# Optimization experiments

Measured on AMD Instinct MI355X. Metric: run time of the kernel, lower is better.

## Reference

```python
import jax, jax.numpy as jnp
import numpy as np

HID, H, D, DFF = 128, 4, 128, 2048   # hidden_dim, nheads, out_feats per head, dim_feedforward
N, E, B = 32768, 524288, 32
EPS = 1e-5
SLOPE = 0.2  # DGL EdgeGATConv negative_slope default


def setup_inputs() -> dict:
    key = jax.random.key(0)
    ks = jax.random.split(key, 16)
    s = 0.05
    return {
        "h": jax.random.normal(ks[0], (N, HID), jnp.float32),
        "e": jax.random.normal(ks[1], (E, 1), jnp.float32),
        "src": jax.random.randint(ks[2], (E,), 0, N, jnp.int32),
        "dst": jax.random.randint(ks[3], (E,), 0, N, jnp.int32),
        "batch_size": B,
        # EdgeGATConv params (fc / fc_edge / res_fc are bias-free in DGL)
        "W_fc": jax.random.normal(ks[4], (HID, H * D), jnp.float32) * s,
        "attn_l": jax.random.normal(ks[5], (H, D), jnp.float32) * s,
        "attn_r": jax.random.normal(ks[6], (H, D), jnp.float32) * s,
        "W_fe": jax.random.normal(ks[7], (1, H * D), jnp.float32) * s,
        "attn_e": jax.random.normal(ks[8], (H, D), jnp.float32) * s,
        "W_res": jax.random.normal(ks[9], (HID, H * D), jnp.float32) * s,
        "gat_bias": jnp.zeros((H * D,), jnp.float32),
        # linear_mha + norms + FFN
        "W_mha": jax.random.normal(ks[10], (H * D, HID), jnp.float32) * s,
        "b_mha": jnp.zeros((HID,), jnp.float32),
        "n1_g": jnp.ones((HID,), jnp.float32),
        "n1_b": jnp.zeros((HID,), jnp.float32),
        "n2_g": jnp.ones((HID,), jnp.float32),
        "n2_b": jnp.zeros((HID,), jnp.float32),
        "W1": jax.random.normal(ks[11], (HID, DFF), jnp.float32) * s,
        "b1": jnp.zeros((DFF,), jnp.float32),
        "W2": jax.random.normal(ks[12], (DFF, HID), jnp.float32) * s,
        "b2": jnp.zeros((HID,), jnp.float32),
    }


def _ln(x, g, b):
    mu = x.mean(-1, keepdims=True)
    var = ((x - mu) ** 2).mean(-1, keepdims=True)
    return (x - mu) * jax.lax.rsqrt(var + EPS) * g + b


def reference(h, e, src, dst, batch_size, W_fc, attn_l, attn_r, W_fe, attn_e,
              W_res, gat_bias, W_mha, b_mha, n1_g, n1_b, n2_g, n2_b,
              W1, b1, W2, b2):
    n = h.shape[0]
    h0 = h
    # --- EdgeGATConv (eval mode: dropouts are identity) ---
    ft = (h @ W_fc).reshape(n, H, D)                         # (N,H,D)
    el = jnp.einsum("nhd,hd->nh", ft, attn_l)                # (N,H)
    er = jnp.einsum("nhd,hd->nh", ft, attn_r)
    fe = (e @ W_fe).reshape(-1, H, D)                        # (E,H,D)
    ee = jnp.einsum("ehd,hd->eh", fe, attn_e)                # (E,H)
    sc = jax.nn.leaky_relu(el[src] + er[dst] + ee, SLOPE)    # (E,H)
    # segment softmax over incoming edges of each dst node
    m = jax.ops.segment_max(sc, dst, num_segments=n)         # (N,H)
    m = jnp.where(jnp.isfinite(m), m, 0.0)                   # empty segments
    w = jnp.exp(sc - m[dst])
    z = jax.ops.segment_sum(w, dst, num_segments=n)
    zd = z[dst]
    alpha = w / jnp.where(zd == 0, 1.0, zd)                  # (E,H)
    msg = ft[src] * alpha[:, :, None]                        # (E,H,D)
    rst = jax.ops.segment_sum(msg, dst, num_segments=n)      # (N,H,D)
    rst = rst + (h0 @ W_res).reshape(n, H, D) + gat_bias.reshape(1, H, D)
    # --- transformer wrapper ---
    x = jax.nn.relu(rst).reshape(n, H * D)
    x = jax.nn.relu(x @ W_mha + b_mha)
    x = _ln(h0 + x, n1_g, n1_b)
    x = x.reshape(batch_size, -1, x.shape[1])                # (B, N/B, HID)
    ff = jax.nn.relu(x @ W1 + b1) @ W2 + b2
    return _ln(x + ff, n2_g, n2_b)
```

## Files before the change

kernel.cpp:

```cpp
#include <hip/hip_runtime.h>
#include <hip/hip_bf16.h>

#define N_NODES 32768
#define E_EDGES 524288
#define HIDDIM 128
#define FDIM 512
#define DFF 2048
#define LN_EPS 1e-5f
#define SLOPE 0.2f
#define CAP 64

typedef __bf16 bf16_t;
typedef __bf16 bf16x8 __attribute__((ext_vector_type(8)));
typedef float f32x4 __attribute__((ext_vector_type(4)));
typedef float f32x2 __attribute__((ext_vector_type(2)));

#define GLD_LDS16(gp, lp) __builtin_amdgcn_global_load_lds( \
    (const __attribute__((address_space(1))) unsigned int*)(gp), \
    (__attribute__((address_space(3))) unsigned int*)(lp), 16, 0, 0)

__device__ inline unsigned char f32_to_e4m3(float v) {
#if __has_builtin(__builtin_amdgcn_cvt_pk_fp8_f32)
    return (unsigned char)(__builtin_amdgcn_cvt_pk_fp8_f32(v, v, 0, false) & 0xff);
#else
    unsigned bits = __float_as_uint(v);
    unsigned sign = (bits >> 24) & 0x80;
    float av = fabsf(v);
    if (av >= 448.f) return (unsigned char)(sign | 0x7E);
    int e = (int)((bits >> 23) & 0xFF) - 127;
    if (e < -6) { int n = (int)rintf(av * 512.f); return (unsigned char)(sign | n); }
    float ulp = exp2f((float)(e - 3));
    int n = (int)rintf(av / ulp);
    if (n == 16) { e += 1; n = 8; }
    return (unsigned char)(sign | ((e + 7) << 3) | (n - 8));
#endif
}
template<bool HI>
__device__ inline f32x2 e4m3x2_to_f32(unsigned u) {
#if __has_builtin(__builtin_amdgcn_cvt_pk_f32_fp8)
    return __builtin_amdgcn_cvt_pk_f32_fp8(u, HI);
#else
    f32x2 r;
    unsigned b0 = HI ? ((u >> 16) & 0xff) : (u & 0xff);
    unsigned b1 = HI ? ((u >> 24) & 0xff) : ((u >> 8) & 0xff);
    unsigned bs[2] = {b0, b1};
    for (int i = 0; i < 2; ++i) {
        unsigned b = bs[i];
        float s = (b & 0x80) ? -1.f : 1.f;
        int e = (b >> 3) & 15, m = b & 7;
        float v = e ? (8 + m) * exp2f((float)(e - 10)) : m * exp2f(-9.f);
        r[i] = s * v;
    }
    return r;
#endif
}

__device__ inline void pack_range(const float* __restrict__ B, bf16_t* __restrict__ out,
                                  int id, int N) {
    const int g = id / N, n = id % N;
    union { bf16_t b[8]; uint4 u; } pk;
#pragma unroll
    for (int j = 0; j < 8; ++j) pk.b[j] = (bf16_t)B[(size_t)(g * 8 + j) * N + n];
    *(uint4*)(out + (size_t)id * 8) = pk.u;
}

__global__ __launch_bounds__(256) void prep_kernel(const float* __restrict__ h, bf16_t* __restrict__ hb,
                                                   const float* __restrict__ W_fc, bf16_t* __restrict__ Wfc_p,
                                                   const float* __restrict__ W_res, bf16_t* __restrict__ Wres_p,
                                                   const float* __restrict__ W_mha, bf16_t* __restrict__ Wmha_p,
                                                   const float* __restrict__ W1, bf16_t* __restrict__ W1_p,
                                                   const float* __restrict__ W2, bf16_t* __restrict__ W2_p,
                                                   const float* __restrict__ W_fe, const float* __restrict__ attn_e,
                                                   float* __restrict__ ce) {
    int bid = blockIdx.x;
    const int tid = threadIdx.x;
    if (bid < 4096) {
        const int id = bid * 256 + tid;
        const float4 v = ((const float4*)h)[id];
        union { bf16_t b[4]; uint2 u; } pk;
        pk.b[0] = (bf16_t)v.x; pk.b[1] = (bf16_t)v.y; pk.b[2] = (bf16_t)v.z; pk.b[3] = (bf16_t)v.w;
        *(uint2*)(hb + (size_t)id * 4) = pk.u;
        return;
    }
    bid -= 4096;
    if (bid < 32)  { pack_range(W_fc,  Wfc_p,  bid * 256 + tid, 512);  return; }
    bid -= 32;
    if (bid < 32)  { pack_range(W_res, Wres_p, bid * 256 + tid, 512);  return; }
    bid -= 32;
    if (bid < 32)  { pack_range(W_mha, Wmha_p, bid * 256 + tid, 128);  return; }
    bid -= 32;
    if (bid < 128) { pack_range(W1,    W1_p,   bid * 256 + tid, 2048); return; }
    bid -= 128;
    if (bid < 128) { pack_range(W2,    W2_p,   bid * 256 + tid, 128);  return; }
    if (tid < 128) {
        const float4 w = ((const float4*)W_fe)[tid];
        const float4 a = ((const float4*)attn_e)[tid];
        float p = w.x * a.x + w.y * a.y + w.z * a.z + w.w * a.w;
        for (int off = 16; off; off >>= 1) p += __shfl_down(p, off, 32);
        if ((tid & 31) == 0) ce[tid >> 5] = p;
    }
}

__global__ __launch_bounds__(256, 2) void gemm_ftres(const bf16_t* __restrict__ A,
                                                     const bf16_t* __restrict__ Bf,
                                                     const bf16_t* __restrict__ Brs,
                                                     const float* __restrict__ attn_l,
                                                     const float* __restrict__ attn_r,
                                                     unsigned char* __restrict__ ft8,
                                                     float* __restrict__ el,
                                                     float* __restrict__ er,
                                                     bf16_t* __restrict__ res) {
    __shared__ __align__(16) bf16_t lA[4096];
    __shared__ __align__(16) bf16_t lBf[4096];
    __shared__ __align__(16) bf16_t lBr[4096];
    __shared__ float s_el[2][128], s_er[2][128];
    const int tid = threadIdx.x, lane = tid & 63, wave = tid >> 6;
    const int wm = (wave >> 1) * 64, wn = (wave & 1) * 64;
    const int row0 = blockIdx.y * 128;
    const int head = blockIdx.x, col0 = head * 128;
    const int ko = lane >> 4, rl = lane & 15;
    f32x4 accf[4][4] = {};
    f32x4 accr[4][4] = {};
    const int c0 = tid, c1 = tid + 256;
    const int g0 = c0 >> 7, m0 = c0 & 127;
    const int g1 = c1 >> 7, m1 = c1 & 127;
    for (int k0 = 0; k0 < 128; k0 += 32) {
        __syncthreads();
        GLD_LDS16(A + (size_t)(row0 + m0) * 128 + k0 + g0 * 8, lA + c0 * 8);
        GLD_LDS16(A + (size_t)(row0 + m1) * 128 + k0 + g1 * 8, lA + c1 * 8);
        GLD_LDS16(Bf + ((size_t)(k0 / 8 + g0) * 512 + col0 + m0) * 8, lBf + c0 * 8);
        GLD_LDS16(Bf + ((size_t)(k0 / 8 + g1) * 512 + col0 + m1) * 8, lBf + c1 * 8);
        GLD_LDS16(Brs + ((size_t)(k0 / 8 + g0) * 512 + col0 + m0) * 8, lBr + c0 * 8);
        GLD_LDS16(Brs + ((size_t)(k0 / 8 + g1) * 512 + col0 + m1) * 8, lBr + c1 * 8);
        __syncthreads();
        bf16x8 af[4], bff[4], bfr[4];
#pragma unroll
        for (int i = 0; i < 4; ++i) {
            af[i]  = *(const bf16x8*)&lA[(ko * 128 + wm + i * 16 + rl) * 8];
            bff[i] = *(const bf16x8*)&lBf[(ko * 128 + wn + i * 16 + rl) * 8];
            bfr[i] = *(const bf16x8*)&lBr[(ko * 128 + wn + i * 16 + rl) * 8];
        }
#pragma unroll
        for (int i = 0; i < 4; ++i)
#pragma unroll
            for (int j = 0; j < 4; ++j) {
                accf[i][j] = __builtin_amdgcn_mfma_f32_16x16x32_bf16(af[i], bff[j], accf[i][j], 0, 0, 0);
                accr[i][j] = __builtin_amdgcn_mfma_f32_16x16x32_bf16(af[i], bfr[j], accr[i][j], 0, 0, 0);
            }
    }
    const int cr = (lane >> 4) * 4, cc = lane & 15;
    float al[4], ar[4];
#pragma unroll
    for (int j = 0; j < 4; ++j) {
        al[j] = attn_l[col0 + wn + j * 16 + cc];
        ar[j] = attn_r[col0 + wn + j * 16 + cc];
    }
#pragma unroll
    for (int i = 0; i < 4; ++i)
#pragma unroll
        for (int r = 0; r < 4; ++r) {
            const int row = row0 + wm + i * 16 + cr + r;
            float pel = 0.f, per = 0.f;
#pragma unroll
            for (int j = 0; j < 4; ++j) {
                const int col = col0 + wn + j * 16 + cc;
                const float v = accf[i][j][r];
                ft8[(size_t)row * 512 + col] = f32_to_e4m3(v);
                res[(size_t)row * 512 + col] = (bf16_t)accr[i][j][r];
                pel += v * al[j];
                per += v * ar[j];
            }
#pragma unroll
            for (int m = 1; m < 16; m <<= 1) {
                pel += __shfl_xor(pel, m);
                per += __shfl_xor(per, m);
            }
            if (cc == 0) {
                s_el[wn >> 6][wm + i * 16 + cr + r] = pel;
                s_er[wn >> 6][wm + i * 16 + cr + r] = per;
            }
        }
    __syncthreads();
    if (tid < 128) {
        el[(size_t)(row0 + tid) * 4 + head] = s_el[0][tid] + s_el[1][tid];
        er[(size_t)(row0 + tid) * 4 + head] = s_er[0][tid] + s_er[1][tid];
    }
}

__global__ __launch_bounds__(256) void gemm_mha_ln(const bf16_t* __restrict__ A,
                                                   const bf16_t* __restrict__ Bp,
                                                   const float* __restrict__ bias,
                                                   const float* __restrict__ h0,
                                                   const float* __restrict__ gamma,
                                                   const float* __restrict__ beta,
                                                   bf16_t* __restrict__ out) {
    __shared__ __align__(16) bf16_t lA[1024];
    __shared__ __align__(16) bf16_t lB[4096];
    __shared__ float s_s1[4][32], s_s2[4][32], s_mu[32], s_rs[32];
    const int tid = threadIdx.x, lane = tid & 63, wave = tid >> 6;
    const int wn = wave * 32;
    const int row0 = blockIdx.x * 32;
    const int ko = lane >> 4, rl = lane & 15;
    f32x4 acc[2][2] = {};
    for (int k0 = 0; k0 < 512; k0 += 32) {
        __syncthreads();
        if (tid < 128) {
            const int g = tid >> 5, m = tid & 31;
            GLD_LDS16(A + (size_t)(row0 + m) * 512 + k0 + g * 8, lA + tid * 8);
        }
        {
            const int g0 = tid >> 7, n0 = tid & 127;
            GLD_LDS16(Bp + ((size_t)(k0 / 8 + g0) * 128 + n0) * 8, lB + tid * 8);
            const int c1 = tid + 256, g1 = c1 >> 7, n1 = c1 & 127;
            GLD_LDS16(Bp + ((size_t)(k0 / 8 + g1) * 128 + n1) * 8, lB + c1 * 8);
        }
        __syncthreads();
        bf16x8 af[2], bfr[2];
#pragma unroll
        for (int i = 0; i < 2; ++i)
            af[i] = *(const bf16x8*)&lA[(ko * 32 + i * 16 + rl) * 8];
#pragma unroll
        for (int j = 0; j < 2; ++j)
            bfr[j] = *(const bf16x8*)&lB[(ko * 128 + wn + j * 16 + rl) * 8];
#pragma unroll
        for (int i = 0; i < 2; ++i)
#pragma unroll
            for (int j = 0; j < 2; ++j)
                acc[i][j] = __builtin_amdgcn_mfma_f32_16x16x32_bf16(af[i], bfr[j], acc[i][j], 0, 0, 0);
    }
    const int cr = (lane >> 4) * 4, cc = lane & 15;
#pragma unroll
    for (int j = 0; j < 2; ++j) {
        const int col = wn + j * 16 + cc;
        const float bb = bias[col];
#pragma unroll
        for (int i = 0; i < 2; ++i)
#pragma unroll
            for (int r = 0; r < 4; ++r) {
                const int row = row0 + i * 16 + cr + r;
                acc[i][j][r] = fmaxf(acc[i][j][r] + bb, 0.f) + h0[(size_t)row * 128 + col];
            }
    }
#pragma unroll
    for (int i = 0; i < 2; ++i)
#pragma unroll
        for (int r = 0; r < 4; ++r) {
            float s1 = 0.f, s2 = 0.f;
#pragma unroll
            for (int j = 0; j < 2; ++j) { const float v = acc[i][j][r]; s1 += v; s2 += v * v; }
#pragma unroll
            for (int m = 1; m < 16; m <<= 1) {
                s1 += __shfl_xor(s1, m);
                s2 += __shfl_xor(s2, m);
            }
            if (cc == 0) {
                s_s1[wave][i * 16 + cr + r] = s1;
                s_s2[wave][i * 16 + cr + r] = s2;
            }
        }
    __syncthreads();
    if (tid < 32) {
        const float a = s_s1[0][tid] + s_s1[1][tid] + s_s1[2][tid] + s_s1[3][tid];
        const float q = s_s2[0][tid] + s_s2[1][tid] + s_s2[2][tid] + s_s2[3][tid];
        const float mu = a * (1.f / 128.f);
        s_mu[tid] = mu;
        s_rs[tid] = rsqrtf(q * (1.f / 128.f) - mu * mu + LN_EPS);
    }
    __syncthreads();
#pragma unroll
    for (int j = 0; j < 2; ++j) {
        const int col = wn + j * 16 + cc;
        const float gg = gamma[col], bb = beta[col];
#pragma unroll
        for (int i = 0; i < 2; ++i)
#pragma unroll
            for (int r = 0; r < 4; ++r) {
                const int rloc = i * 16 + cr + r;
                out[(size_t)(row0 + rloc) * 128 + col] =
                    (bf16_t)((acc[i][j][r] - s_mu[rloc]) * s_rs[rloc] * gg + bb);
            }
    }
}

__global__ __launch_bounds__(512, 2) void ffn_fused(const bf16_t* __restrict__ x3,
                                                    const bf16_t* __restrict__ W1p,
                                                    const float* __restrict__ b1,
                                                    const bf16_t* __restrict__ W2p,
                                                    const float* __restrict__ b2,
                                                    const float* __restrict__ gamma,
                                                    const float* __restrict__ beta,
                                                    float* __restrict__ out) {
    __shared__ __align__(16) bf16_t lW1[3][8192];
    __shared__ __align__(16) bf16_t lW2[4][8192];
    __shared__ __align__(16) bf16_t lY[2][8192];
    __shared__ float s_s1[2][128], s_s2[2][128], s_mu[128], s_rs[128];
    const int tid = threadIdx.x, lane = tid & 63, wave = tid >> 6;
    const int kh  = wave & 1;
    const int ds  = wave & 3;
    const int cg  = (wave >> 1) & 1;
    const int rg  = wave >> 2;
    const int wr  = rg * 64;
    const int wc1 = ds * 16;
    const int wc2 = cg * 64;
    const int row0 = blockIdx.x * 128;
    const int ko = lane >> 4, rl = lane & 15;
    const int cr = ko * 4, cc = rl;

    bf16_t* lX = &lW1[0][0];
#pragma unroll
    for (int it = 0; it < 4; ++it) {
        const int c = it * 512 + tid, g = c >> 7, m = c & 127;
        GLD_LDS16(x3 + (size_t)(row0 + m) * 128 + g * 8, lX + c * 8);
    }
    __syncthreads();
    bf16x8 afx[4][4];
#pragma unroll
    for (int ir = 0; ir < 4; ++ir)
#pragma unroll
        for (int kk = 0; kk < 4; ++kk)
            afx[ir][kk] = *(const bf16x8*)&lX[((kk * 4 + ko) * 128 + wr + ir * 16 + rl) * 8];
    asm volatile("s_waitcnt lgkmcnt(0)" ::: "memory");
    __builtin_amdgcn_s_barrier();
    __builtin_amdgcn_sched_barrier(0);

    auto stage_chunk = [&](int chn, bf16_t* w1d, bf16_t* w2d) {
#pragma unroll
        for (int it = 0; it < 2; ++it) {
            const int c = it * 512 + tid, g = c >> 6, n = c & 63;
            GLD_LDS16(W1p + ((size_t)g * 2048 + chn * 64 + n) * 8, w1d + c * 8);
        }
#pragma unroll
        for (int it = 0; it < 2; ++it) {
            const int c = it * 512 + tid, g = c >> 7, n = c & 127;
            GLD_LDS16(W2p + ((size_t)(chn * 8 + g) * 128 + n) * 8, w2d + c * 8);
        }
    };

    f32x4 xacc[4][4] = {};

    auto gemm1 = [&](int chn, const bf16_t* w1c, bf16_t* ydst) {
        f32x4 yacc[4] = {};
        __builtin_amdgcn_s_setprio(1);
#pragma unroll
        for (int kk = 0; kk < 4; ++kk) {
            const bf16x8 bw = *(const bf16x8*)&w1c[((kk * 4 + ko) * 64 + wc1 + rl) * 8];
#pragma unroll
            for (int ir = 0; ir < 4; ++ir)
                yacc[ir] = __builtin_amdgcn_mfma_f32_16x16x32_bf16(bw, afx[ir][kk], yacc[ir], 0, 0, 0);
        }
        __builtin_amdgcn_s_setprio(0);
        const int dffb = wc1 + cr;
        const float4 bb = *(const float4*)(b1 + chn * 64 + dffb);
#pragma unroll
        for (int ir = 0; ir < 4; ++ir) {
            const int rowx = wr + ir * 16 + cc;
            union { bf16_t b[4]; uint2 u; } pk;
            pk.b[0] = (bf16_t)fmaxf(yacc[ir][0] + bb.x, 0.f);
            pk.b[1] = (bf16_t)fmaxf(yacc[ir][1] + bb.y, 0.f);
            pk.b[2] = (bf16_t)fmaxf(yacc[ir][2] + bb.z, 0.f);
            pk.b[3] = (bf16_t)fmaxf(yacc[ir][3] + bb.w, 0.f);
            *(uint2*)&ydst[((dffb >> 3) * 128 + rowx) * 8 + (dffb & 7)] = pk.u;
        }
    };

    auto gemm2 = [&](const bf16_t* w2c, const bf16_t* ysrc) {
        bf16x8 ay[4], bw2[4];
#pragma unroll
        for (int ir = 0; ir < 4; ++ir)
            ay[ir] = *(const bf16x8*)&ysrc[((kh * 4 + ko) * 128 + wr + ir * 16 + rl) * 8];
#pragma unroll
        for (int j = 0; j < 4; ++j)
            bw2[j] = *(const bf16x8*)&w2c[((kh * 4 + ko) * 128 + wc2 + j * 16 + rl) * 8];
        __builtin_amdgcn_s_setprio(1);
#pragma unroll
        for (int ir = 0; ir < 4; ++ir)
#pragma unroll
            for (int j = 0; j < 4; ++j)
                xacc[ir][j] = __builtin_amdgcn_mfma_f32_16x16x32_bf16(ay[ir], bw2[j], xacc[ir][j], 0, 0, 0);
        __builtin_amdgcn_s_setprio(0);
    };

#pragma unroll
    for (int pc = 0; pc < 2; ++pc)
        stage_chunk(pc, lW1[pc], lW2[pc]);
    asm volatile("s_waitcnt vmcnt(4)" ::: "memory");
    __builtin_amdgcn_s_barrier();
    __builtin_amdgcn_sched_barrier(0);

    stage_chunk(2, lW1[2], lW2[2]);
    gemm1(0, lW1[0], lY[0]);
    __builtin_amdgcn_sched_barrier(0);
    asm volatile("s_waitcnt vmcnt(4) lgkmcnt(0)" ::: "memory");
    __builtin_amdgcn_s_barrier();
    __builtin_amdgcn_sched_barrier(0);

    int r1 = 1, sb1 = 0, r2 = 0, sb2 = 3, p = 1;
#pragma unroll 1
    for (int i = 1; i < 32; ++i) {
        if (i < 30)
            stage_chunk(i + 2, lW1[sb1], lW2[sb2]);
        gemm1(i, lW1[r1], lY[p]);
        gemm2(lW2[r2], lY[p ^ 1]);
        __builtin_amdgcn_sched_barrier(0);
        if (i < 30)
            asm volatile("s_waitcnt vmcnt(4) lgkmcnt(0)" ::: "memory");
        else if (i == 30)
            asm volatile("s_waitcnt vmcnt(2) lgkmcnt(0)" ::: "memory");
        else
            asm volatile("s_waitcnt vmcnt(0) lgkmcnt(0)" ::: "memory");
        __builtin_amdgcn_s_barrier();
        __builtin_amdgcn_sched_barrier(0);
        r1 = (r1 == 2) ? 0 : r1 + 1;
        sb1 = (sb1 == 2) ? 0 : sb1 + 1;
        r2 = (r2 == 3) ? 0 : r2 + 1;
        sb2 = (sb2 == 3) ? 0 : sb2 + 1;
        p ^= 1;
    }
    gemm2(lW2[3], lY[1]);

    __syncthreads();
    {
        const int q = (wave >> 1) & 3;
        float* scr = (q < 2) ? ((float*)&lW1[0][0] + q * 4352)
                             : ((float*)&lW2[0][0] + (q - 2) * 4352);
        if (kh) {
#pragma unroll
            for (int ir = 0; ir < 4; ++ir)
#pragma unroll
                for (int j = 0; j < 4; ++j)
                    *(f32x4*)(scr + lane * 68 + (ir * 4 + j) * 4) = xacc[ir][j];
        }
        __syncthreads();
        if (!kh) {
#pragma unroll
            for (int ir = 0; ir < 4; ++ir)
#pragma unroll
                for (int j = 0; j < 4; ++j)
                    xacc[ir][j] += *(const f32x4*)(scr + lane * 68 + (ir * 4 + j) * 4);
        }
    }

    if (!kh) {
#pragma unroll
        for (int j = 0; j < 4; ++j) {
            const int col = wc2 + j * 16 + cc;
            const float bb = b2[col];
#pragma unroll
            for (int ir = 0; ir < 4; ++ir)
#pragma unroll
                for (int r = 0; r < 4; ++r) {
                    const int row = wr + ir * 16 + cr + r;
                    xacc[ir][j][r] += bb + (float)x3[(size_t)(row0 + row) * 128 + col];
                }
        }
#pragma unroll
        for (int ir = 0; ir < 4; ++ir)
#pragma unroll
            for (int r = 0; r < 4; ++r) {
                float s1v = 0.f, s2v = 0.f;
#pragma unroll
                for (int j = 0; j < 4; ++j) { const float v = xacc[ir][j][r]; s1v += v; s2v += v * v; }
#pragma unroll
                for (int m = 1; m < 16; m <<= 1) {
                    s1v += __shfl_xor(s1v, m);
                    s2v += __shfl_xor(s2v, m);
                }
                if (cc == 0) {
                    s_s1[cg][wr + ir * 16 + cr + r] = s1v;
                    s_s2[cg][wr + ir * 16 + cr + r] = s2v;
                }
            }
    }
    __syncthreads();
    if (tid < 128) {
        const float a = s_s1[0][tid] + s_s1[1][tid];
        const float q = s_s2[0][tid] + s_s2[1][tid];
        const float mu = a * (1.f / 128.f);
        s_mu[tid] = mu;
        s_rs[tid] = rsqrtf(q * (1.f / 128.f) - mu * mu + LN_EPS);
    }
    __syncthreads();
    if (!kh) {
#pragma unroll
        for (int j = 0; j < 4; ++j) {
            const int col = wc2 + j * 16 + cc;
            const float gg = gamma[col], bb = beta[col];
#pragma unroll
            for (int ir = 0; ir < 4; ++ir)
#pragma unroll
                for (int r = 0; r < 4; ++r) {
                    const int rloc = wr + ir * 16 + cr + r;
                    out[(size_t)(row0 + rloc) * 128 + col] =
                        (xacc[ir][j][r] - s_mu[rloc]) * s_rs[rloc] * gg + bb;
                }
        }
    }
}

__global__ __launch_bounds__(256) void edge_build(const float* __restrict__ evals,
                                                  const int* __restrict__ src,
                                                  const int* __restrict__ dst,
                                                  const float* __restrict__ el,
                                                  const float* __restrict__ er,
                                                  const float* __restrict__ ce,
                                                  int* __restrict__ cursor,
                                                  int* __restrict__ csr_src,
                                                  float4* __restrict__ csr_w) {
    const int e = blockIdx.x * 256 + threadIdx.x;
    const int s = src[e], d = dst[e];
    const float ev = evals[e];
    const float4 l = *(const float4*)(el + (size_t)s * 4);
    const float4 r = *(const float4*)(er + (size_t)d * 4);
    const float4 c = *(const float4*)ce;
    float4 w;
    {
        float v;
        v = l.x + r.x + ev * c.x; v = v >= 0.f ? v : SLOPE * v; w.x = __expf(v);
        v = l.y + r.y + ev * c.y; v = v >= 0.f ? v : SLOPE * v; w.y = __expf(v);
        v = l.z + r.z + ev * c.z; v = v >= 0.f ? v : SLOPE * v; w.z = __expf(v);
        v = l.w + r.w + ev * c.w; v = v >= 0.f ? v : SLOPE * v; w.w = __expf(v);
    }
    const int pos = atomicAdd(&cursor[d], 1);
    if (pos < CAP) {
        csr_src[(size_t)d * CAP + pos] = s;
        csr_w[(size_t)d * CAP + pos] = w;
    }
}

__global__ __launch_bounds__(128) void aggregate_kernel(const unsigned char* __restrict__ ft8,
                                                        const bf16_t* __restrict__ res,
                                                        const int* __restrict__ cursor,
                                                        const int* __restrict__ csr_src,
                                                        const float4* __restrict__ csr_w,
                                                        const float* __restrict__ gat_bias,
                                                        bf16_t* __restrict__ x1) {
    const int n = blockIdx.x, t = threadIdx.x;
    __shared__ int s_src[CAP];
    __shared__ float s_w[CAP][4];
    const int deg = min(cursor[n], CAP);
    const int ht = t >> 5;
    if (t < deg) {
        s_src[t] = csr_src[(size_t)n * CAP + t];
        *(float4*)s_w[t] = csr_w[(size_t)n * CAP + t];
    }
    __syncthreads();
    float4 acc = {0.f, 0.f, 0.f, 0.f};
    float z = 0.f;
    int j = 0;
    for (; j + 4 <= deg; j += 4) {
        const float w0 = s_w[j + 0][ht], w1 = s_w[j + 1][ht];
        const float w2 = s_w[j + 2][ht], w3 = s_w[j + 3][ht];
        const unsigned u0 = *(const unsigned*)(ft8 + (size_t)s_src[j + 0] * 512 + t * 4);
        const unsigned u1 = *(const unsigned*)(ft8 + (size_t)s_src[j + 1] * 512 + t * 4);
        const unsigned u2 = *(const unsigned*)(ft8 + (size_t)s_src[j + 2] * 512 + t * 4);
        const unsigned u3 = *(const unsigned*)(ft8 + (size_t)s_src[j + 3] * 512 + t * 4);
        z += (w0 + w1) + (w2 + w3);
        {
            const f32x2 lo = e4m3x2_to_f32<false>(u0), hi = e4m3x2_to_f32<true>(u0);
            acc.x += w0 * lo[0]; acc.y += w0 * lo[1]; acc.z += w0 * hi[0]; acc.w += w0 * hi[1];
        }
        {
            const f32x2 lo = e4m3x2_to_f32<false>(u1), hi = e4m3x2_to_f32<true>(u1);
            acc.x += w1 * lo[0]; acc.y += w1 * lo[1]; acc.z += w1 * hi[0]; acc.w += w1 * hi[1];
        }
        {
            const f32x2 lo = e4m3x2_to_f32<false>(u2), hi = e4m3x2_to_f32<true>(u2);
            acc.x += w2 * lo[0]; acc.y += w2 * lo[1]; acc.z += w2 * hi[0]; acc.w += w2 * hi[1];
        }
        {
            const f32x2 lo = e4m3x2_to_f32<false>(u3), hi = e4m3x2_to_f32<true>(u3);
            acc.x += w3 * lo[0]; acc.y += w3 * lo[1]; acc.z += w3 * hi[0]; acc.w += w3 * hi[1];
        }
    }
    for (; j < deg; ++j) {
        const float w = s_w[j][ht];
        z += w;
        const unsigned u = *(const unsigned*)(ft8 + (size_t)s_src[j] * 512 + t * 4);
        const f32x2 lo = e4m3x2_to_f32<false>(u);
        const f32x2 hi = e4m3x2_to_f32<true>(u);
        acc.x += w * lo[0]; acc.y += w * lo[1];
        acc.z += w * hi[0]; acc.w += w * hi[1];
    }
    const float rz = deg > 0 ? 1.f / z : 0.f;
    const uint2 ur = *(const uint2*)(res + (size_t)n * FDIM + t * 4);
    const float4 gb = ((const float4*)gat_bias)[t];
    union { bf16_t b[4]; uint2 u; } pk;
    pk.b[0] = (bf16_t)fmaxf(acc.x * rz + __uint_as_float(ur.x << 16) + gb.x, 0.f);
    pk.b[1] = (bf16_t)fmaxf(acc.y * rz + __uint_as_float(ur.x & 0xFFFF0000u) + gb.y, 0.f);
    pk.b[2] = (bf16_t)fmaxf(acc.z * rz + __uint_as_float(ur.y << 16) + gb.z, 0.f);
    pk.b[3] = (bf16_t)fmaxf(acc.w * rz + __uint_as_float(ur.y & 0xFFFF0000u) + gb.w, 0.f);
    *(uint2*)(x1 + (size_t)n * FDIM + t * 4) = pk.u;
}

extern "C" void kernel_launch(void* const* d_in, const int* in_sizes, int n_in,
                              void* d_out, int out_size, void* d_ws, size_t ws_size,
                              hipStream_t stream) {
    const float* h        = (const float*)d_in[0];
    const float* evals    = (const float*)d_in[1];
    const int*   src      = (const int*)d_in[2];
    const int*   dst      = (const int*)d_in[3];
    const float* W_fc     = (const float*)d_in[5];
    const float* attn_l   = (const float*)d_in[6];
    const float* attn_r   = (const float*)d_in[7];
    const float* W_fe     = (const float*)d_in[8];
    const float* attn_e   = (const float*)d_in[9];
    const float* W_res    = (const float*)d_in[10];
    const float* gat_bias = (const float*)d_in[11];
    const float* W_mha    = (const float*)d_in[12];
    const float* b_mha    = (const float*)d_in[13];
    const float* n1_g     = (const float*)d_in[14];
    const float* n1_b     = (const float*)d_in[15];
    const float* n2_g     = (const float*)d_in[16];
    const float* n2_b     = (const float*)d_in[17];
    const float* W1       = (const float*)d_in[18];
    const float* b1       = (const float*)d_in[19];
    const float* W2       = (const float*)d_in[20];
    const float* b2       = (const float*)d_in[21];

    char* ws = (char*)d_ws;
    unsigned char* ft8 = (unsigned char*)(ws + 0);
    bf16_t* res     = (bf16_t*)(ws + 16777216ull);
    bf16_t* x1      = (bf16_t*)(ws + 50331648ull);
    float4* csr_w   = (float4*)(ws + 83886080ull);
    int*    csr_src = (int*)   (ws + 117440512ull);
    bf16_t* x3b     = (bf16_t*)(ws + 125829120ull);
    bf16_t* hb      = (bf16_t*)(ws + 134217728ull);
    bf16_t* Wfc_p   = (bf16_t*)(ws + 142606336ull);
    bf16_t* Wres_p  = (bf16_t*)(ws + 142737408ull);
    bf16_t* Wmha_p  = (bf16_t*)(ws + 142868480ull);
    bf16_t* W1_p    = (bf16_t*)(ws + 142999552ull);
    bf16_t* W2_p    = (bf16_t*)(ws + 143523840ull);
    float*  el      = (float*) (ws + 144048128ull);
    float*  er      = (float*) (ws + 144572416ull);
    float*  ce      = (float*) (ws + 145096704ull);
    int*    cursor  = (int*)   (ws + 145096768ull);

    if (ws_size < 146000000ull) return;

    (void)hipMemsetAsync(cursor, 0, 131072, stream);

    prep_kernel<<<4449, 256, 0, stream>>>(h, hb, W_fc, Wfc_p, W_res, Wres_p,
                                          W_mha, Wmha_p, W1, W1_p, W2, W2_p,
                                          W_fe, attn_e, ce);
    gemm_ftres<<<dim3(4, 256), 256, 0, stream>>>(hb, Wfc_p, Wres_p, attn_l, attn_r, ft8, el, er, res);
    edge_build<<<E_EDGES / 256, 256, 0, stream>>>(evals, src, dst, el, er, ce, cursor, csr_src, csr_w);
    aggregate_kernel<<<N_NODES, 128, 0, stream>>>(ft8, res, cursor, csr_src, csr_w, gat_bias, x1);
    gemm_mha_ln<<<1024, 256, 0, stream>>>(x1, Wmha_p, b_mha, h, n1_g, n1_b, x3b);
    ffn_fused<<<256, 512, 0, stream>>>(x3b, W1_p, b1, W2_p, b2, n2_g, n2_b, (float*)d_out);
}
```

Measured before the change: 296.9 us.

## Fuse neighbor aggregation into MHA GEMM+LN and pack CSR records

Merges the per-node aggregation kernel with the linear_mha GEMM and LayerNorm, so each 64-row block aggregates its nodes into LDS as bf16 and feeds them straight into MFMA. This removes the x1 intermediate round trip through global memory and one launch. The CSR is also packed into a single 16-byte record per edge holding fp16 attention weights and the source index, replacing two separate arrays. In exchange, the aggregation phase gets only 512 blocks with a serial 32-row loop per half-block and no LDS staging of edge records. The 64 KB LDS footprint per block also limits occupancy, and fp16 weights add a small precision change.

```diff
diff --git a/kernel.cpp b/kernel.cpp
--- a/kernel.cpp
+++ b/kernel.cpp
@@ -1,5 +1,6 @@
 #include <hip/hip_runtime.h>
 #include <hip/hip_bf16.h>
+#include <hip/hip_fp16.h>
 
 #define N_NODES 32768
 #define E_EDGES 524288
@@ -187,101 +188,6 @@
     }
 }
 
-__global__ __launch_bounds__(256) void gemm_mha_ln(const bf16_t* __restrict__ A,
-                                                   const bf16_t* __restrict__ Bp,
-                                                   const float* __restrict__ bias,
-                                                   const float* __restrict__ h0,
-                                                   const float* __restrict__ gamma,
-                                                   const float* __restrict__ beta,
-                                                   bf16_t* __restrict__ out) {
-    __shared__ __align__(16) bf16_t lA[1024];
-    __shared__ __align__(16) bf16_t lB[4096];
-    __shared__ float s_s1[4][32], s_s2[4][32], s_mu[32], s_rs[32];
-    const int tid = threadIdx.x, lane = tid & 63, wave = tid >> 6;
-    const int wn = wave * 32;
-    const int row0 = blockIdx.x * 32;
-    const int ko = lane >> 4, rl = lane & 15;
-    f32x4 acc[2][2] = {};
-    for (int k0 = 0; k0 < 512; k0 += 32) {
-        __syncthreads();
-        if (tid < 128) {
-            const int g = tid >> 5, m = tid & 31;
-            GLD_LDS16(A + (size_t)(row0 + m) * 512 + k0 + g * 8, lA + tid * 8);
-        }
-        {
-            const int g0 = tid >> 7, n0 = tid & 127;
-            GLD_LDS16(Bp + ((size_t)(k0 / 8 + g0) * 128 + n0) * 8, lB + tid * 8);
-            const int c1 = tid + 256, g1 = c1 >> 7, n1 = c1 & 127;
-            GLD_LDS16(Bp + ((size_t)(k0 / 8 + g1) * 128 + n1) * 8, lB + c1 * 8);
-        }
-        __syncthreads();
-        bf16x8 af[2], bfr[2];
-#pragma unroll
-        for (int i = 0; i < 2; ++i)
-            af[i] = *(const bf16x8*)&lA[(ko * 32 + i * 16 + rl) * 8];
-#pragma unroll
-        for (int j = 0; j < 2; ++j)
-            bfr[j] = *(const bf16x8*)&lB[(ko * 128 + wn + j * 16 + rl) * 8];
-#pragma unroll
-        for (int i = 0; i < 2; ++i)
-#pragma unroll
-            for (int j = 0; j < 2; ++j)
-                acc[i][j] = __builtin_amdgcn_mfma_f32_16x16x32_bf16(af[i], bfr[j], acc[i][j], 0, 0, 0);
-    }
-    const int cr = (lane >> 4) * 4, cc = lane & 15;
-#pragma unroll
-    for (int j = 0; j < 2; ++j) {
-        const int col = wn + j * 16 + cc;
-        const float bb = bias[col];
-#pragma unroll
-        for (int i = 0; i < 2; ++i)
-#pragma unroll
-            for (int r = 0; r < 4; ++r) {
-                const int row = row0 + i * 16 + cr + r;
-                acc[i][j][r] = fmaxf(acc[i][j][r] + bb, 0.f) + h0[(size_t)row * 128 + col];
-            }
-    }
-#pragma unroll
-    for (int i = 0; i < 2; ++i)
-#pragma unroll
-        for (int r = 0; r < 4; ++r) {
-            float s1 = 0.f, s2 = 0.f;
-#pragma unroll
-            for (int j = 0; j < 2; ++j) { const float v = acc[i][j][r]; s1 += v; s2 += v * v; }
-#pragma unroll
-            for (int m = 1; m < 16; m <<= 1) {
-                s1 += __shfl_xor(s1, m);
-                s2 += __shfl_xor(s2, m);
-            }
-            if (cc == 0) {
-                s_s1[wave][i * 16 + cr + r] = s1;
-                s_s2[wave][i * 16 + cr + r] = s2;
-            }
-        }
-    __syncthreads();
-    if (tid < 32) {
-        const float a = s_s1[0][tid] + s_s1[1][tid] + s_s1[2][tid] + s_s1[3][tid];
-        const float q = s_s2[0][tid] + s_s2[1][tid] + s_s2[2][tid] + s_s2[3][tid];
-        const float mu = a * (1.f / 128.f);
-        s_mu[tid] = mu;
-        s_rs[tid] = rsqrtf(q * (1.f / 128.f) - mu * mu + LN_EPS);
-    }
-    __syncthreads();
-#pragma unroll
-    for (int j = 0; j < 2; ++j) {
-        const int col = wn + j * 16 + cc;
-        const float gg = gamma[col], bb = beta[col];
-#pragma unroll
-        for (int i = 0; i < 2; ++i)
-#pragma unroll
-            for (int r = 0; r < 4; ++r) {
-                const int rloc = i * 16 + cr + r;
-                out[(size_t)(row0 + rloc) * 128 + col] =
-                    (bf16_t)((acc[i][j][r] - s_mu[rloc]) * s_rs[rloc] * gg + bb);
-            }
-    }
-}
-
 __global__ __launch_bounds__(512, 2) void ffn_fused(const bf16_t* __restrict__ x3,
                                                     const bf16_t* __restrict__ W1p,
                                                     const float* __restrict__ b1,
@@ -504,8 +410,7 @@
                                                   const float* __restrict__ er,
                                                   const float* __restrict__ ce,
                                                   int* __restrict__ cursor,
-                                                  int* __restrict__ csr_src,
-                                                  float4* __restrict__ csr_w) {
+                                                  uint4* __restrict__ csr) {
     const int e = blockIdx.x * 256 + threadIdx.x;
     const int s = src[e], d = dst[e];
     const float ev = evals[e];
@@ -522,74 +427,169 @@
     }
     const int pos = atomicAdd(&cursor[d], 1);
     if (pos < CAP) {
-        csr_src[(size_t)d * CAP + pos] = s;
-        csr_w[(size_t)d * CAP + pos] = w;
-    }
-}
-
-__global__ __launch_bounds__(128) void aggregate_kernel(const unsigned char* __restrict__ ft8,
-                                                        const bf16_t* __restrict__ res,
-                                                        const int* __restrict__ cursor,
-                                                        const int* __restrict__ csr_src,
-                                                        const float4* __restrict__ csr_w,
-                                                        const float* __restrict__ gat_bias,
-                                                        bf16_t* __restrict__ x1) {
-    const int n = blockIdx.x, t = threadIdx.x;
-    __shared__ int s_src[CAP];
-    __shared__ float s_w[CAP][4];
-    const int deg = min(cursor[n], CAP);
-    const int ht = t >> 5;
-    if (t < deg) {
-        s_src[t] = csr_src[(size_t)n * CAP + t];
-        *(float4*)s_w[t] = csr_w[(size_t)n * CAP + t];
-    }
-    __syncthreads();
-    float4 acc = {0.f, 0.f, 0.f, 0.f};
-    float z = 0.f;
-    int j = 0;
-    for (; j + 4 <= deg; j += 4) {
-        const float w0 = s_w[j + 0][ht], w1 = s_w[j + 1][ht];
-        const float w2 = s_w[j + 2][ht], w3 = s_w[j + 3][ht];
-        const unsigned u0 = *(const unsigned*)(ft8 + (size_t)s_src[j + 0] * 512 + t * 4);
-        const unsigned u1 = *(const unsigned*)(ft8 + (size_t)s_src[j + 1] * 512 + t * 4);
-        const unsigned u2 = *(const unsigned*)(ft8 + (size_t)s_src[j + 2] * 512 + t * 4);
-        const unsigned u3 = *(const unsigned*)(ft8 + (size_t)s_src[j + 3] * 512 + t * 4);
-        z += (w0 + w1) + (w2 + w3);
+        uint4 rec;
+        rec.x = (unsigned)__half_as_ushort(__float2half(w.x)) |
+                ((unsigned)__half_as_ushort(__float2half(w.y)) << 16);
+        rec.y = (unsigned)__half_as_ushort(__float2half(w.z)) |
+                ((unsigned)__half_as_ushort(__float2half(w.w)) << 16);
+        rec.z = (unsigned)s;
+        rec.w = 0u;
+        csr[(size_t)d * CAP + pos] = rec;
+    }
+}
+
+__device__ inline float w_of(const uint4& rec, int ht) {
+    const unsigned pair = (ht < 2) ? rec.x : rec.y;
+    const unsigned sh = (ht & 1) ? (pair >> 16) : (pair & 0xffffu);
+    return __half2float(__ushort_as_half((unsigned short)sh));
+}
+
+__global__ __launch_bounds__(256, 2) void agg_mha_ln(const unsigned char* __restrict__ ft8,
+                                                     const bf16_t* __restrict__ res,
+                                                     const int* __restrict__ cursor,
+                                                     const uint4* __restrict__ csr,
+                                                     const float* __restrict__ gat_bias,
+                                                     const bf16_t* __restrict__ Bp,
+                                                     const float* __restrict__ bias,
+                                                     const float* __restrict__ h0,
+                                                     const float* __restrict__ gamma,
+                                                     const float* __restrict__ beta,
+                                                     bf16_t* __restrict__ out) {
+    __shared__ __align__(16) bf16_t lX[64 * 512];
+    __shared__ __align__(16) bf16_t lB[4096];
+    __shared__ float s_s1[4][64], s_s2[4][64], s_mu[64], s_rs[64];
+    const int tid = threadIdx.x;
+    const int row0 = blockIdx.x * 64;
+
+    {
+        const int half = tid >> 7;
+        const int t = tid & 127;
+        const int ht = t >> 5;
+        const float4 gb = ((const float4*)gat_bias)[t];
+        for (int r = 0; r < 32; ++r) {
+            const int n = row0 + r * 2 + half;
+            const int deg = min(cursor[n], CAP);
+            const uint4* rec = csr + (size_t)n * CAP;
+            float4 acc = {0.f, 0.f, 0.f, 0.f};
+            float z = 0.f;
+            int j = 0;
+            for (; j + 4 <= deg; j += 4) {
+                const uint4 r0 = rec[j], r1 = rec[j + 1], r2 = rec[j + 2], r3 = rec[j + 3];
+                const unsigned u0 = *(const unsigned*)(ft8 + (size_t)r0.z * 512 + t * 4);
+                const unsigned u1 = *(const unsigned*)(ft8 + (size_t)r1.z * 512 + t * 4);
+                const unsigned u2 = *(const unsigned*)(ft8 + (size_t)r2.z * 512 + t * 4);
+                const unsigned u3 = *(const unsigned*)(ft8 + (size_t)r3.z * 512 + t * 4);
+                const float w0 = w_of(r0, ht), w1 = w_of(r1, ht);
+                const float w2 = w_of(r2, ht), w3 = w_of(r3, ht);
+                z += (w0 + w1) + (w2 + w3);
+                { const f32x2 lo = e4m3x2_to_f32<false>(u0), hi = e4m3x2_to_f32<true>(u0);
+                  acc.x += w0 * lo[0]; acc.y += w0 * lo[1]; acc.z += w0 * hi[0]; acc.w += w0 * hi[1]; }
+                { const f32x2 lo = e4m3x2_to_f32<false>(u1), hi = e4m3x2_to_f32<true>(u1);
+                  acc.x += w1 * lo[0]; acc.y += w1 * lo[1]; acc.z += w1 * hi[0]; acc.w += w1 * hi[1]; }
+                { const f32x2 lo = e4m3x2_to_f32<false>(u2), hi = e4m3x2_to_f32<true>(u2);
+                  acc.x += w2 * lo[0]; acc.y += w2 * lo[1]; acc.z += w2 * hi[0]; acc.w += w2 * hi[1]; }
+                { const f32x2 lo = e4m3x2_to_f32<false>(u3), hi = e4m3x2_to_f32<true>(u3);
+                  acc.x += w3 * lo[0]; acc.y += w3 * lo[1]; acc.z += w3 * hi[0]; acc.w += w3 * hi[1]; }
+            }
+            for (; j < deg; ++j) {
+                const uint4 r0 = rec[j];
+                const float w = w_of(r0, ht);
+                z += w;
+                const unsigned u = *(const unsigned*)(ft8 + (size_t)r0.z * 512 + t * 4);
+                const f32x2 lo = e4m3x2_to_f32<false>(u), hi = e4m3x2_to_f32<true>(u);
+                acc.x += w * lo[0]; acc.y += w * lo[1];
+                acc.z += w * hi[0]; acc.w += w * hi[1];
+            }
+            const float rz = deg > 0 ? 1.f / z : 0.f;
+            const uint2 ur = *(const uint2*)(res + (size_t)n * FDIM + t * 4);
+            union { bf16_t b[4]; uint2 u; } pk;
+            pk.b[0] = (bf16_t)fmaxf(acc.x * rz + __uint_as_float(ur.x << 16) + gb.x, 0.f);
+            pk.b[1] = (bf16_t)fmaxf(acc.y * rz + __uint_as_float(ur.x & 0xFFFF0000u) + gb.y, 0.f);
+            pk.b[2] = (bf16_t)fmaxf(acc.z * rz + __uint_as_float(ur.y << 16) + gb.z, 0.f);
+            pk.b[3] = (bf16_t)fmaxf(acc.w * rz + __uint_as_float(ur.y & 0xFFFF0000u) + gb.w, 0.f);
+            *(uint2*)&lX[(((t >> 1) * 64) + (r * 2 + half)) * 8 + (t & 1) * 4] = pk.u;
+        }
+    }
+    __syncthreads();
+
+    const int lane = tid & 63, wave = tid >> 6;
+    const int wn = wave * 32;
+    const int ko = lane >> 4, rl = lane & 15;
+    f32x4 acc2[4][2] = {};
+    for (int k0 = 0; k0 < 512; k0 += 32) {
+        __syncthreads();
         {
-            const f32x2 lo = e4m3x2_to_f32<false>(u0), hi = e4m3x2_to_f32<true>(u0);
-            acc.x += w0 * lo[0]; acc.y += w0 * lo[1]; acc.z += w0 * hi[0]; acc.w += w0 * hi[1];
-        }
-        {
-            const f32x2 lo = e4m3x2_to_f32<false>(u1), hi = e4m3x2_to_f32<true>(u1);
-            acc.x += w1 * lo[0]; acc.y += w1 * lo[1]; acc.z += w1 * hi[0]; acc.w += w1 * hi[1];
-        }
-        {
-            const f32x2 lo = e4m3x2_to_f32<false>(u2), hi = e4m3x2_to_f32<true>(u2);
-            acc.x += w2 * lo[0]; acc.y += w2 * lo[1]; acc.z += w2 * hi[0]; acc.w += w2 * hi[1];
-        }
-        {
-            const f32x2 lo = e4m3x2_to_f32<false>(u3), hi = e4m3x2_to_f32<true>(u3);
-            acc.x += w3 * lo[0]; acc.y += w3 * lo[1]; acc.z += w3 * hi[0]; acc.w += w3 * hi[1];
-        }
-    }
-    for (; j < deg; ++j) {
-        const float w = s_w[j][ht];
-        z += w;
-        const unsigned u = *(const unsigned*)(ft8 + (size_t)s_src[j] * 512 + t * 4);
-        const f32x2 lo = e4m3x2_to_f32<false>(u);
-        const f32x2 hi = e4m3x2_to_f32<true>(u);
-        acc.x += w * lo[0]; acc.y += w * lo[1];
-        acc.z += w * hi[0]; acc.w += w * hi[1];
-    }
-    const float rz = deg > 0 ? 1.f / z : 0.f;
-    const uint2 ur = *(const uint2*)(res + (size_t)n * FDIM + t * 4);
-    const float4 gb = ((const float4*)gat_bias)[t];
-    union { bf16_t b[4]; uint2 u; } pk;
-    pk.b[0] = (bf16_t)fmaxf(acc.x * rz + __uint_as_float(ur.x << 16) + gb.x, 0.f);
-    pk.b[1] = (bf16_t)fmaxf(acc.y * rz + __uint_as_float(ur.x & 0xFFFF0000u) + gb.y, 0.f);
-    pk.b[2] = (bf16_t)fmaxf(acc.z * rz + __uint_as_float(ur.y << 16) + gb.z, 0.f);
-    pk.b[3] = (bf16_t)fmaxf(acc.w * rz + __uint_as_float(ur.y & 0xFFFF0000u) + gb.w, 0.f);
-    *(uint2*)(x1 + (size_t)n * FDIM + t * 4) = pk.u;
+            const int c0 = tid, g0 = c0 >> 7, n0 = c0 & 127;
+            GLD_LDS16(Bp + ((size_t)(k0 / 8 + g0) * 128 + n0) * 8, lB + c0 * 8);
+            const int c1 = tid + 256, g1 = c1 >> 7, n1 = c1 & 127;
+            GLD_LDS16(Bp + ((size_t)(k0 / 8 + g1) * 128 + n1) * 8, lB + c1 * 8);
+        }
+        __syncthreads();
+        bf16x8 af[4], bfr[2];
+#pragma unroll
+        for (int i = 0; i < 4; ++i)
+            af[i] = *(const bf16x8*)&lX[(((k0 >> 3) + ko) * 64 + i * 16 + rl) * 8];
+#pragma unroll
+        for (int j = 0; j < 2; ++j)
+            bfr[j] = *(const bf16x8*)&lB[(ko * 128 + wn + j * 16 + rl) * 8];
+#pragma unroll
+        for (int i = 0; i < 4; ++i)
+#pragma unroll
+            for (int j = 0; j < 2; ++j)
+                acc2[i][j] = __builtin_amdgcn_mfma_f32_16x16x32_bf16(af[i], bfr[j], acc2[i][j], 0, 0, 0);
+    }
+    const int cr = (lane >> 4) * 4, cc = lane & 15;
+#pragma unroll
+    for (int j = 0; j < 2; ++j) {
+        const int col = wn + j * 16 + cc;
+        const float bb = bias[col];
+#pragma unroll
+        for (int i = 0; i < 4; ++i)
+#pragma unroll
+            for (int r = 0; r < 4; ++r) {
+                const int row = row0 + i * 16 + cr + r;
+                acc2[i][j][r] = fmaxf(acc2[i][j][r] + bb, 0.f) + h0[(size_t)row * 128 + col];
+            }
+    }
+#pragma unroll
+    for (int i = 0; i < 4; ++i)
+#pragma unroll
+        for (int r = 0; r < 4; ++r) {
+            float s1 = 0.f, s2 = 0.f;
+#pragma unroll
+            for (int j = 0; j < 2; ++j) { const float v = acc2[i][j][r]; s1 += v; s2 += v * v; }
+#pragma unroll
+            for (int m = 1; m < 16; m <<= 1) {
+                s1 += __shfl_xor(s1, m);
+                s2 += __shfl_xor(s2, m);
+            }
+            if (cc == 0) {
+                s_s1[wave][i * 16 + cr + r] = s1;
+                s_s2[wave][i * 16 + cr + r] = s2;
+            }
+        }
+    __syncthreads();
+    if (tid < 64) {
+        const float a = s_s1[0][tid] + s_s1[1][tid] + s_s1[2][tid] + s_s1[3][tid];
+        const float q = s_s2[0][tid] + s_s2[1][tid] + s_s2[2][tid] + s_s2[3][tid];
+        const float mu = a * (1.f / 128.f);
+        s_mu[tid] = mu;
+        s_rs[tid] = rsqrtf(q * (1.f / 128.f) - mu * mu + LN_EPS);
+    }
+    __syncthreads();
+#pragma unroll
+    for (int j = 0; j < 2; ++j) {
+        const int col = wn + j * 16 + cc;
+        const float gg = gamma[col], bb = beta[col];
+#pragma unroll
+        for (int i = 0; i < 4; ++i)
+#pragma unroll
+            for (int r = 0; r < 4; ++r) {
+                const int rloc = i * 16 + cr + r;
+                out[(size_t)(row0 + rloc) * 128 + col] =
+                    (bf16_t)((acc2[i][j][r] - s_mu[rloc]) * s_rs[rloc] * gg + bb);
+            }
+    }
 }
 
 extern "C" void kernel_launch(void* const* d_in, const int* in_sizes, int n_in,
@@ -620,9 +620,7 @@
     char* ws = (char*)d_ws;
     unsigned char* ft8 = (unsigned char*)(ws + 0);
     bf16_t* res     = (bf16_t*)(ws + 16777216ull);
-    bf16_t* x1      = (bf16_t*)(ws + 50331648ull);
-    float4* csr_w   = (float4*)(ws + 83886080ull);
-    int*    csr_src = (int*)   (ws + 117440512ull);
+    uint4*  csr     = (uint4*) (ws + 83886080ull);
     bf16_t* x3b     = (bf16_t*)(ws + 125829120ull);
     bf16_t* hb      = (bf16_t*)(ws + 134217728ull);
     bf16_t* Wfc_p   = (bf16_t*)(ws + 142606336ull);
@@ -643,8 +641,8 @@
                                           W_mha, Wmha_p, W1, W1_p, W2, W2_p,
                                           W_fe, attn_e, ce);
     gemm_ftres<<<dim3(4, 256), 256, 0, stream>>>(hb, Wfc_p, Wres_p, attn_l, attn_r, ft8, el, er, res);
-    edge_build<<<E_EDGES / 256, 256, 0, stream>>>(evals, src, dst, el, er, ce, cursor, csr_src, csr_w);
-    aggregate_kernel<<<N_NODES, 128, 0, stream>>>(ft8, res, cursor, csr_src, csr_w, gat_bias, x1);
-    gemm_mha_ln<<<1024, 256, 0, stream>>>(x1, Wmha_p, b_mha, h, n1_g, n1_b, x3b);
+    edge_build<<<E_EDGES / 256, 256, 0, stream>>>(evals, src, dst, el, er, ce, cursor, csr);
+    agg_mha_ln<<<512, 256, 0, stream>>>(ft8, res, cursor, csr, gat_bias,
+                                        Wmha_p, b_mha, h, n1_g, n1_b, x3b);
     ffn_fused<<<256, 512, 0, stream>>>(x3b, W1_p, b1, W2_p, b2, n2_g, n2_b, (float*)d_out);
 }
```

Result: slower. 369.2 us (+24.3%).
